# Kernel optimization log

Hardware: AMD Instinct MI355X
Metric: run time of the kernel (lower is better)

Reference implementation:

```python
import jax, jax.numpy as jnp
import numpy as np

HEAD_SIZE = 12
INNER_DIM = 64
BIG_NEG = 1e12


def _sinusoidal(seq_len, dim):
    # interleaved [sin, cos, sin, cos, ...] like SinusoidalPositionEmbedding('zero')
    pos = jnp.arange(seq_len, dtype=jnp.float32)
    inv = jnp.power(10000.0, -2.0 * jnp.arange(dim // 2, dtype=jnp.float32) / dim)
    ang = pos[:, None] * inv[None, :]                       # (L, dim/2)
    return jnp.stack([jnp.sin(ang), jnp.cos(ang)], axis=-1).reshape(seq_len, dim)


def _rope_rotate(x, cos_pos, sin_pos):
    # x: (B, L, H, D); rotate-half per interleaved RoPE
    x2 = jnp.stack([-x[..., 1::2], x[..., ::2]], axis=-1).reshape(x.shape)
    return x * cos_pos + x2 * sin_pos


def setup_inputs() -> dict:
    key = jax.random.key(0)
    k1, k2 = jax.random.split(key)
    B, L, HID = 16, 512, 768
    sequence_output = jax.random.normal(k1, (B, L, HID), dtype=jnp.float32)
    mask = jnp.ones((B, L), dtype=jnp.float32)
    W = jax.random.normal(k2, (HID, HEAD_SIZE * INNER_DIM * 2), dtype=jnp.float32) * 0.02
    b = jnp.zeros((HEAD_SIZE * INNER_DIM * 2,), dtype=jnp.float32)
    return {"sequence_output": sequence_output, "mask": mask, "W": W, "b": b}


def reference(sequence_output, mask, W, b):
    B, L, _ = sequence_output.shape
    H, D = HEAD_SIZE, INNER_DIM
    out = sequence_output @ W + b                           # (B, L, H*2D)
    out = out.reshape(B, L, H, 2 * D)
    qw, kw = out[..., :D], out[..., D:]                     # (B, L, H, D)
    pos = _sinusoidal(L, D)                                 # (L, D)
    cos_pos = jnp.repeat(pos[:, None, 1::2], 2, axis=-1)    # (L, 1, D)
    sin_pos = jnp.repeat(pos[:, None, ::2], 2, axis=-1)
    qw = _rope_rotate(qw, cos_pos, sin_pos)
    kw = _rope_rotate(kw, cos_pos, sin_pos)
    logits = jnp.einsum('bmhd,bnhd->bhmn', qw, kw)          # (B, H, L, L)
    pad = mask[:, None, None, :]                            # (B, 1, 1, L)
    logits = logits * pad - (1.0 - pad) * BIG_NEG
    tril = jnp.tril(jnp.ones((L, L), dtype=logits.dtype), -1)
    logits = logits - tril * BIG_NEG
    return logits / (D ** 0.5)
```

## Files before the change

### kernel.cpp

```cpp
#include <hip/hip_runtime.h>
#include <stdint.h>

typedef float f32x4 __attribute__((ext_vector_type(4)));

#define HEADS 12
#define DDIM 64
#define LSEQ 512
#define HID 768
#define NOUT 1536
#define BIG_NEG 1000000000000.0f

__device__ __forceinline__ void gl_lds16(const void* g, void* l) {
    __builtin_amdgcn_global_load_lds(
        (const __attribute__((address_space(1))) void*)g,
        (__attribute__((address_space(3))) void*)l, 16, 0, 0);
}

__device__ __forceinline__ void ldsbar() {
    asm volatile("s_waitcnt lgkmcnt(0)" ::: "memory");
    __builtin_amdgcn_s_barrier();
}

__device__ __forceinline__ uint32_t pk4_fp8(float a, float b, float c, float d) {
    uint32_t v = __builtin_amdgcn_cvt_pk_fp8_f32(a, b, 0, false);
    v = __builtin_amdgcn_cvt_pk_fp8_f32(c, d, v, true);
    return v;
}

__global__ __launch_bounds__(256) void prep_k(
    const float* __restrict__ X, const float* __restrict__ W,
    uint8_t* __restrict__ Xq, uint8_t* __restrict__ Wtq,
    float* __restrict__ cosT, float* __restrict__ sinT) {

    int blk = blockIdx.x;
    if (blk < 3072) {
        size_t idx = ((size_t)blk * 256 + threadIdx.x) * 8;
        float4 f0 = *(const float4*)(X + idx);
        float4 f1 = *(const float4*)(X + idx + 4);
        uint2 p;
        p.x = pk4_fp8(f0.x, f0.y, f0.z, f0.w);
        p.y = pk4_fp8(f1.x, f1.y, f1.z, f1.w);
        *(uint2*)(Xq + idx) = p;
    } else if (blk < 4224) {
        __shared__ float Ls[32][33];
        int b2 = blk - 3072;
        int n0 = (b2 % 48) * 32, k0 = (b2 / 48) * 32;
        int tx = threadIdx.x & 31, ty = threadIdx.x >> 5;
#pragma unroll
        for (int rr = 0; rr < 4; ++rr) {
            int k = ty + rr * 8;
            Ls[k][tx] = W[(size_t)(k0 + k) * NOUT + n0 + tx];
        }
        __syncthreads();
        int n = threadIdx.x >> 3, c = threadIdx.x & 7;
        uint32_t w = pk4_fp8(Ls[4*c][n], Ls[4*c+1][n], Ls[4*c+2][n], Ls[4*c+3][n]);
        *(uint32_t*)(Wtq + (size_t)(n0 + n) * HID + k0 + c * 4) = w;
    } else {
        int idx = (blk - 4224) * 256 + threadIdx.x;
        int l = idx >> 6, d = idx & 63;
        int p = d >> 1;
        float inv = powf(10000.0f, (-2.0f * (float)p) / 64.0f);
        float ang = (float)l * inv;
        cosT[idx] = cosf(ang);
        sinT[idx] = sinf(ang);
    }
}

__global__ __launch_bounds__(256) void proj_rope_k(
    const uint8_t* __restrict__ Xq, const uint8_t* __restrict__ Wtq,
    const float* __restrict__ bias, const float* __restrict__ cosT,
    const float* __restrict__ sinT,
    uint8_t* __restrict__ qq, uint8_t* __restrict__ kq) {

    __shared__ __align__(16) uint8_t As[128 * 64];
    __shared__ __align__(16) uint8_t Bs[128 * 64];

    const int tid = threadIdx.x;
    const int m0 = blockIdx.x * 128, n0 = blockIdx.y * 128;
    const int lane = tid & 63, wid = tid >> 6;
    const int wm = wid >> 1, wn = wid & 1;
    const int lr = lane & 15, kg = lane >> 4;

    const int srow = tid >> 2, sc = tid & 3;

    f32x4 acc[4][4] = {};

    for (int k0 = 0; k0 < HID; k0 += 64) {
#pragma unroll
        for (int j = 0; j < 2; ++j) {
            int r = j * 64 + srow;
            int cs = sc ^ ((r >> 1) & 3);
            gl_lds16(Wtq + (size_t)(n0 + r) * HID + k0 + cs * 16,
                     Bs + j * 4096 + tid * 16);
            gl_lds16(Xq + (size_t)(m0 + r) * HID + k0 + cs * 16,
                     As + j * 4096 + tid * 16);
        }
        __syncthreads();
#pragma unroll
        for (int ks = 0; ks < 2; ++ks) {
            unsigned long long af[4], xf[4];
#pragma unroll
            for (int ai = 0; ai < 4; ++ai) {
                int row = wn * 64 + ai * 16 + lr;
                int sl = (ks * 4 + kg) ^ (row & 6);
                af[ai] = *(const unsigned long long*)(Bs + row * 64 + sl * 8);
            }
#pragma unroll
            for (int bi = 0; bi < 4; ++bi) {
                int row = wm * 64 + bi * 16 + lr;
                int sl = (ks * 4 + kg) ^ (row & 6);
                xf[bi] = *(const unsigned long long*)(As + row * 64 + sl * 8);
            }
#pragma unroll
            for (int ai = 0; ai < 4; ++ai)
#pragma unroll
                for (int bi = 0; bi < 4; ++bi)
                    acc[ai][bi] = __builtin_amdgcn_mfma_f32_16x16x32_fp8_fp8(
                        (long long)af[ai], (long long)xf[bi], acc[ai][bi], 0, 0, 0);
        }
        __syncthreads();
    }

#pragma unroll
    for (int ai = 0; ai < 4; ++ai) {
        int nb = n0 + wn * 64 + ai * 16 + kg * 4;
        int h = nb >> 7, d2 = nb & 127;
        int d = d2 & 63;
        uint8_t* dst = (d2 >= 64) ? kq : qq;
        float4 b4 = *(const float4*)&bias[nb];
#pragma unroll
        for (int bi = 0; bi < 4; ++bi) {
            int m = m0 + wm * 64 + bi * 16 + lr;
            int bidx = m >> 9, lpos = m & 511;
            float4 c4 = *(const float4*)&cosT[lpos * 64 + d];
            float4 s4 = *(const float4*)&sinT[lpos * 64 + d];
            float v0 = acc[ai][bi][0] + b4.x;
            float v1 = acc[ai][bi][1] + b4.y;
            float v2 = acc[ai][bi][2] + b4.z;
            float v3 = acc[ai][bi][3] + b4.w;
            float o0 = v0 * c4.x - v1 * s4.x;
            float o1 = v1 * c4.y + v0 * s4.y;
            float o2 = v2 * c4.z - v3 * s4.z;
            float o3 = v3 * c4.w + v2 * s4.w;
            uint32_t pw = pk4_fp8(o0, o1, o2, o3);
            *(uint32_t*)(dst + (((size_t)bidx * HEADS + h) * LSEQ + lpos) * DDIM + d) = pw;
        }
    }
}

__global__ __launch_bounds__(256) void attn_k(
    const uint8_t* __restrict__ qq, const uint8_t* __restrict__ kq,
    const float* __restrict__ mask, float* __restrict__ out) {

    __shared__ __align__(16) uint8_t Qs[8192];
    __shared__ __align__(16) uint8_t Ks[8192];
    __shared__ __align__(16) float Es[32 * 132];
    __shared__ int wok[4];

    const int tid = threadIdx.x;
    const int bh = blockIdx.y;
    const int mtile = blockIdx.x;
    const int m0 = mtile * 128;
    const int lane = tid & 63, wid = tid >> 6;
    const int wm = wid >> 1, wn = wid & 1;
    const int lr = lane & 15, kg = lane >> 4;
    const int b = bh / HEADS;

    int myok = 1;
    for (int c0 = tid; c0 < m0; c0 += 256)
        myok &= (mask[b * LSEQ + c0] == 1.0f) ? 1 : 0;
    unsigned long long bal = __ballot(myok);
    if (lane == 0) wok[wid] = (bal == ~0ull) ? 1 : 0;
    ldsbar();
    const int nstart = (wok[0] & wok[1] & wok[2] & wok[3]) ? mtile : 0;

    const uint8_t* qbase = qq + ((size_t)bh * LSEQ + m0) * DDIM;
    const uint8_t* kbase = kq + (size_t)bh * LSEQ * DDIM;

    const int srow = tid >> 2, sc = tid & 3;
#pragma unroll
    for (int j = 0; j < 2; ++j) {
        int r = j * 64 + srow;
        int cs = sc ^ ((r >> 1) & 3);
        gl_lds16(qbase + (size_t)r * DDIM + cs * 16, Qs + j * 4096 + tid * 16);
        gl_lds16(kbase + (size_t)(nstart * 128 + r) * DDIM + cs * 16,
                 Ks + j * 4096 + tid * 16);
    }
    __syncthreads();

    const int colb = (tid & 31) * 4;
    const int rrow = tid >> 5;
    float* obase = out + (size_t)bh * LSEQ * LSEQ;

    for (int nt = nstart; nt < 4; ++nt) {
        f32x4 acc[4][4] = {};
#pragma unroll
        for (int ks = 0; ks < 2; ++ks) {
            unsigned long long af[4], qf[4];
#pragma unroll
            for (int ai = 0; ai < 4; ++ai) {
                int row = wn * 64 + ai * 16 + lr;
                int sl = (ks * 4 + kg) ^ (row & 6);
                af[ai] = *(const unsigned long long*)(Ks + row * 64 + sl * 8);
            }
#pragma unroll
            for (int bi = 0; bi < 4; ++bi) {
                int row = wm * 64 + bi * 16 + lr;
                int sl = (ks * 4 + kg) ^ (row & 6);
                qf[bi] = *(const unsigned long long*)(Qs + row * 64 + sl * 8);
            }
#pragma unroll
            for (int ai = 0; ai < 4; ++ai)
#pragma unroll
                for (int bi = 0; bi < 4; ++bi)
                    acc[ai][bi] = __builtin_amdgcn_mfma_f32_16x16x32_fp8_fp8(
                        (long long)af[ai], (long long)qf[bi], acc[ai][bi], 0, 0, 0);
        }
        ldsbar();

        const int n0 = nt * 128;
        const float4 p4 = *(const float4*)&mask[b * LSEQ + n0 + colb];

        if (nt < 3) {
#pragma unroll
            for (int j = 0; j < 2; ++j) {
                int r = j * 64 + srow;
                int cs = sc ^ ((r >> 1) & 3);
                gl_lds16(kbase + (size_t)((nt + 1) * 128 + r) * DDIM + cs * 16,
                         Ks + j * 4096 + tid * 16);
            }
        }

#pragma unroll
        for (int p = 0; p < 4; ++p) {
            ldsbar();
            if (wm == (p >> 1)) {
                const int bi0 = (p & 1) * 2;
#pragma unroll
                for (int bb = 0; bb < 2; ++bb) {
                    int bi = bi0 + bb;
                    int row = bb * 16 + lr;
#pragma unroll
                    for (int ai = 0; ai < 4; ++ai) {
                        int n = wn * 64 + ai * 16 + kg * 4;
                        *(f32x4*)&Es[row * 132 + n] = acc[ai][bi];
                    }
                }
            }
            ldsbar();
#pragma unroll
            for (int j = 0; j < 4; ++j) {
                int rloc = rrow + j * 8;
                int m = m0 + p * 32 + rloc;
                f32x4 v = *(f32x4*)&Es[rloc * 132 + colb];
                int n = n0 + colb;
                f32x4 o;
                o[0] = (v[0] * p4.x - (1.0f - p4.x) * BIG_NEG
                        - ((m > n + 0) ? BIG_NEG : 0.0f)) * 0.125f;
                o[1] = (v[1] * p4.y - (1.0f - p4.y) * BIG_NEG
                        - ((m > n + 1) ? BIG_NEG : 0.0f)) * 0.125f;
                o[2] = (v[2] * p4.z - (1.0f - p4.z) * BIG_NEG
                        - ((m > n + 2) ? BIG_NEG : 0.0f)) * 0.125f;
                o[3] = (v[3] * p4.w - (1.0f - p4.w) * BIG_NEG
                        - ((m > n + 3) ? BIG_NEG : 0.0f)) * 0.125f;
                __builtin_nontemporal_store(o, (f32x4*)&obase[(size_t)m * LSEQ + n]);
            }
        }

        if (nt < 3) {
            asm volatile("s_waitcnt vmcnt(16) lgkmcnt(0)" ::: "memory");
            __builtin_amdgcn_s_barrier();
        }
    }

    const float CONSTV = (-BIG_NEG) * 0.125f;
    f32x4 cv = {CONSTV, CONSTV, CONSTV, CONSTV};
    for (int nt2 = 0; nt2 < nstart; ++nt2) {
        int n = nt2 * 128 + colb;
#pragma unroll
        for (int p = 0; p < 4; ++p)
#pragma unroll
            for (int j = 0; j < 4; ++j) {
                int m = m0 + p * 32 + rrow + j * 8;
                __builtin_nontemporal_store(cv, (f32x4*)&obase[(size_t)m * LSEQ + n]);
            }
    }
}

extern "C" void kernel_launch(void* const* d_in, const int* in_sizes, int n_in,
                              void* d_out, int out_size, void* d_ws, size_t ws_size,
                              hipStream_t stream) {
    const float* X    = (const float*)d_in[0];
    const float* mask = (const float*)d_in[1];
    const float* W    = (const float*)d_in[2];
    const float* bias = (const float*)d_in[3];
    float* out = (float*)d_out;

    char* ws = (char*)d_ws;
    float*   cosT = (float*)ws;
    float*   sinT = (float*)(ws + 131072);
    uint8_t* Wtq  = (uint8_t*)(ws + 262144);
    uint8_t* Xq   = (uint8_t*)(ws + 1441792);
    uint8_t* qq   = (uint8_t*)(ws + 7733248);
    uint8_t* kq   = (uint8_t*)(ws + 14024704);

    prep_k<<<4352, 256, 0, stream>>>(X, W, Xq, Wtq, cosT, sinT);
    proj_rope_k<<<dim3(64, 12), 256, 0, stream>>>(Xq, Wtq, bias, cosT, sinT, qq, kq);
    attn_k<<<dim3(4, 192), 256, 0, stream>>>(qq, kq, mask, out);
}
```

Before: 86.63 us.

## Double-buffer projection GEMM and retile attention into 64-row blocks with remapped grid

The projection kernel now double-buffers its LDS tiles, prefetching the next K-slice while the MFMAs run on the current one. The attention kernel is retiled to 64 query rows per block, giving 1536 blocks with an XCD-aware index remap. Q fragments are loaded straight into registers instead of LDS, mask rows are preloaded, and the epilogue constants are folded into one FMA with a rotated Es layout to cut bank conflicts. The aim is better latency hiding and occupancy on the output-bandwidth-bound attention store, at the cost of more blocks, each reloading K tiles.

```diff
diff --git a/kernel.cpp b/kernel.cpp
--- a/kernel.cpp
+++ b/kernel.cpp
@@ -2,6 +2,7 @@
 #include <stdint.h>
 
 typedef float f32x4 __attribute__((ext_vector_type(4)));
+typedef unsigned long long u64;
 
 #define HEADS 12
 #define DDIM 64
@@ -9,6 +10,7 @@
 #define HID 768
 #define NOUT 1536
 #define BIG_NEG 1000000000000.0f
+#define BIGS 125000000000.0f
 
 __device__ __forceinline__ void gl_lds16(const void* g, void* l) {
     __builtin_amdgcn_global_load_lds(
@@ -72,8 +74,8 @@
     const float* __restrict__ sinT,
     uint8_t* __restrict__ qq, uint8_t* __restrict__ kq) {
 
-    __shared__ __align__(16) uint8_t As[128 * 64];
-    __shared__ __align__(16) uint8_t Bs[128 * 64];
+    __shared__ __align__(16) uint8_t As[2][128 * 64];
+    __shared__ __align__(16) uint8_t Bs[2][128 * 64];
 
     const int tid = threadIdx.x;
     const int m0 = blockIdx.x * 128, n0 = blockIdx.y * 128;
@@ -85,31 +87,47 @@
 
     f32x4 acc[4][4] = {};
 
-    for (int k0 = 0; k0 < HID; k0 += 64) {
-#pragma unroll
-        for (int j = 0; j < 2; ++j) {
-            int r = j * 64 + srow;
-            int cs = sc ^ ((r >> 1) & 3);
-            gl_lds16(Wtq + (size_t)(n0 + r) * HID + k0 + cs * 16,
-                     Bs + j * 4096 + tid * 16);
-            gl_lds16(Xq + (size_t)(m0 + r) * HID + k0 + cs * 16,
-                     As + j * 4096 + tid * 16);
-        }
-        __syncthreads();
+#pragma unroll
+    for (int j = 0; j < 2; ++j) {
+        int r = j * 64 + srow;
+        int cs = sc ^ ((r >> 1) & 3);
+        gl_lds16(Wtq + (size_t)(n0 + r) * HID + cs * 16, Bs[0] + j * 4096 + tid * 16);
+        gl_lds16(Xq  + (size_t)(m0 + r) * HID + cs * 16, As[0] + j * 4096 + tid * 16);
+    }
+
+    for (int it = 0; it < 12; ++it) {
+        const int cur = it & 1;
+        if (it < 11) {
+            const int k0 = (it + 1) * 64;
+#pragma unroll
+            for (int j = 0; j < 2; ++j) {
+                int r = j * 64 + srow;
+                int cs = sc ^ ((r >> 1) & 3);
+                gl_lds16(Wtq + (size_t)(n0 + r) * HID + k0 + cs * 16,
+                         Bs[cur ^ 1] + j * 4096 + tid * 16);
+                gl_lds16(Xq  + (size_t)(m0 + r) * HID + k0 + cs * 16,
+                         As[cur ^ 1] + j * 4096 + tid * 16);
+            }
+            asm volatile("s_waitcnt vmcnt(4)" ::: "memory");
+        } else {
+            asm volatile("s_waitcnt vmcnt(0)" ::: "memory");
+        }
+        __builtin_amdgcn_s_barrier();
+
 #pragma unroll
         for (int ks = 0; ks < 2; ++ks) {
-            unsigned long long af[4], xf[4];
+            u64 af[4], xf[4];
 #pragma unroll
             for (int ai = 0; ai < 4; ++ai) {
                 int row = wn * 64 + ai * 16 + lr;
                 int sl = (ks * 4 + kg) ^ (row & 6);
-                af[ai] = *(const unsigned long long*)(Bs + row * 64 + sl * 8);
+                af[ai] = *(const u64*)(Bs[cur] + row * 64 + sl * 8);
             }
 #pragma unroll
             for (int bi = 0; bi < 4; ++bi) {
                 int row = wm * 64 + bi * 16 + lr;
                 int sl = (ks * 4 + kg) ^ (row & 6);
-                xf[bi] = *(const unsigned long long*)(As + row * 64 + sl * 8);
+                xf[bi] = *(const u64*)(As[cur] + row * 64 + sl * 8);
             }
 #pragma unroll
             for (int ai = 0; ai < 4; ++ai)
@@ -118,7 +136,7 @@
                     acc[ai][bi] = __builtin_amdgcn_mfma_f32_16x16x32_fp8_fp8(
                         (long long)af[ai], (long long)xf[bi], acc[ai][bi], 0, 0, 0);
         }
-        __syncthreads();
+        ldsbar();
     }
 
 #pragma unroll
@@ -148,31 +166,31 @@
     }
 }
 
-__global__ __launch_bounds__(256) void attn_k(
+__global__ __launch_bounds__(256, 5) void attn_k(
     const uint8_t* __restrict__ qq, const uint8_t* __restrict__ kq,
     const float* __restrict__ mask, float* __restrict__ out) {
 
-    __shared__ __align__(16) uint8_t Qs[8192];
     __shared__ __align__(16) uint8_t Ks[8192];
     __shared__ __align__(16) float Es[32 * 132];
     __shared__ int wok[4];
 
     const int tid = threadIdx.x;
-    const int bh = blockIdx.y;
-    const int mtile = blockIdx.x;
-    const int m0 = mtile * 128;
-    const int lane = tid & 63, wid = tid >> 6;
-    const int wm = wid >> 1, wn = wid & 1;
+    const int bid = blockIdx.x;
+    const int L = (bid & 7) * 192 + (bid >> 3);
+    const int bh = L >> 3;
+    const int m0 = (L & 7) * 64;
+    const int lane = tid & 63, wn = tid >> 6;
     const int lr = lane & 15, kg = lane >> 4;
     const int b = bh / HEADS;
 
+    const int lim = m0 & ~127;
     int myok = 1;
-    for (int c0 = tid; c0 < m0; c0 += 256)
+    for (int c0 = tid; c0 < lim; c0 += 256)
         myok &= (mask[b * LSEQ + c0] == 1.0f) ? 1 : 0;
     unsigned long long bal = __ballot(myok);
-    if (lane == 0) wok[wid] = (bal == ~0ull) ? 1 : 0;
+    if (lane == 0) wok[wn] = (bal == ~0ull) ? 1 : 0;
     ldsbar();
-    const int nstart = (wok[0] & wok[1] & wok[2] & wok[3]) ? mtile : 0;
+    const int nstart = (wok[0] & wok[1] & wok[2] & wok[3]) ? (m0 >> 7) : 0;
 
     const uint8_t* qbase = qq + ((size_t)bh * LSEQ + m0) * DDIM;
     const uint8_t* kbase = kq + (size_t)bh * LSEQ * DDIM;
@@ -182,44 +200,48 @@
     for (int j = 0; j < 2; ++j) {
         int r = j * 64 + srow;
         int cs = sc ^ ((r >> 1) & 3);
-        gl_lds16(qbase + (size_t)r * DDIM + cs * 16, Qs + j * 4096 + tid * 16);
         gl_lds16(kbase + (size_t)(nstart * 128 + r) * DDIM + cs * 16,
                  Ks + j * 4096 + tid * 16);
     }
-    __syncthreads();
+
+    u64 qf[2][4];
+#pragma unroll
+    for (int ks = 0; ks < 2; ++ks)
+#pragma unroll
+        for (int bi = 0; bi < 4; ++bi)
+            qf[ks][bi] = *(const u64*)(qbase + (size_t)(bi * 16 + lr) * DDIM
+                                       + (ks * 4 + kg) * 8);
 
     const int colb = (tid & 31) * 4;
     const int rrow = tid >> 5;
+    float4 mrow[4];
+#pragma unroll
+    for (int t = 0; t < 4; ++t)
+        mrow[t] = *(const float4*)&mask[b * LSEQ + t * 128 + colb];
+
+    __syncthreads();
+
     float* obase = out + (size_t)bh * LSEQ * LSEQ;
 
     for (int nt = nstart; nt < 4; ++nt) {
-        f32x4 acc[4][4] = {};
+        f32x4 acc[2][4] = {};
 #pragma unroll
         for (int ks = 0; ks < 2; ++ks) {
-            unsigned long long af[4], qf[4];
-#pragma unroll
-            for (int ai = 0; ai < 4; ++ai) {
-                int row = wn * 64 + ai * 16 + lr;
+            u64 af[2];
+#pragma unroll
+            for (int ai = 0; ai < 2; ++ai) {
+                int row = wn * 32 + ai * 16 + lr;
                 int sl = (ks * 4 + kg) ^ (row & 6);
-                af[ai] = *(const unsigned long long*)(Ks + row * 64 + sl * 8);
-            }
-#pragma unroll
-            for (int bi = 0; bi < 4; ++bi) {
-                int row = wm * 64 + bi * 16 + lr;
-                int sl = (ks * 4 + kg) ^ (row & 6);
-                qf[bi] = *(const unsigned long long*)(Qs + row * 64 + sl * 8);
-            }
-#pragma unroll
-            for (int ai = 0; ai < 4; ++ai)
+                af[ai] = *(const u64*)(Ks + row * 64 + sl * 8);
+            }
+#pragma unroll
+            for (int ai = 0; ai < 2; ++ai)
 #pragma unroll
                 for (int bi = 0; bi < 4; ++bi)
                     acc[ai][bi] = __builtin_amdgcn_mfma_f32_16x16x32_fp8_fp8(
-                        (long long)af[ai], (long long)qf[bi], acc[ai][bi], 0, 0, 0);
+                        (long long)af[ai], (long long)qf[ks][bi], acc[ai][bi], 0, 0, 0);
         }
         ldsbar();
-
-        const int n0 = nt * 128;
-        const float4 p4 = *(const float4*)&mask[b * LSEQ + n0 + colb];
 
         if (nt < 3) {
 #pragma unroll
@@ -231,57 +253,56 @@
             }
         }
 
-#pragma unroll
-        for (int p = 0; p < 4; ++p) {
-            ldsbar();
-            if (wm == (p >> 1)) {
-                const int bi0 = (p & 1) * 2;
-#pragma unroll
-                for (int bb = 0; bb < 2; ++bb) {
-                    int bi = bi0 + bb;
-                    int row = bb * 16 + lr;
-#pragma unroll
-                    for (int ai = 0; ai < 4; ++ai) {
-                        int n = wn * 64 + ai * 16 + kg * 4;
-                        *(f32x4*)&Es[row * 132 + n] = acc[ai][bi];
-                    }
+        const float4 p4 = mrow[nt];
+        f32x4 ca = {p4.x * 0.125f, p4.y * 0.125f, p4.z * 0.125f, p4.w * 0.125f};
+        f32x4 cb = {(p4.x - 1.0f) * BIGS, (p4.y - 1.0f) * BIGS,
+                    (p4.z - 1.0f) * BIGS, (p4.w - 1.0f) * BIGS};
+        const int n0 = nt * 128;
+
+#pragma unroll
+        for (int p2 = 0; p2 < 2; ++p2) {
+#pragma unroll
+            for (int bb = 0; bb < 2; ++bb) {
+                int bi = p2 * 2 + bb;
+                int row = bb * 16 + lr;
+#pragma unroll
+                for (int ai = 0; ai < 2; ++ai) {
+                    int n = wn * 32 + ai * 16 + kg * 4;
+                    int nc = (n + row * 4) & 127;
+                    *(f32x4*)&Es[row * 132 + nc] = acc[ai][bi];
                 }
             }
             ldsbar();
 #pragma unroll
             for (int j = 0; j < 4; ++j) {
                 int rloc = rrow + j * 8;
-                int m = m0 + p * 32 + rloc;
-                f32x4 v = *(f32x4*)&Es[rloc * 132 + colb];
+                int nc = (colb + rloc * 4) & 127;
+                f32x4 v = *(f32x4*)&Es[rloc * 132 + nc];
+                int m = m0 + p2 * 32 + rloc;
                 int n = n0 + colb;
                 f32x4 o;
-                o[0] = (v[0] * p4.x - (1.0f - p4.x) * BIG_NEG
-                        - ((m > n + 0) ? BIG_NEG : 0.0f)) * 0.125f;
-                o[1] = (v[1] * p4.y - (1.0f - p4.y) * BIG_NEG
-                        - ((m > n + 1) ? BIG_NEG : 0.0f)) * 0.125f;
-                o[2] = (v[2] * p4.z - (1.0f - p4.z) * BIG_NEG
-                        - ((m > n + 2) ? BIG_NEG : 0.0f)) * 0.125f;
-                o[3] = (v[3] * p4.w - (1.0f - p4.w) * BIG_NEG
-                        - ((m > n + 3) ? BIG_NEG : 0.0f)) * 0.125f;
+#pragma unroll
+                for (int i = 0; i < 4; ++i)
+                    o[i] = v[i] * ca[i] + cb[i] - ((m > n + i) ? BIGS : 0.0f);
                 __builtin_nontemporal_store(o, (f32x4*)&obase[(size_t)m * LSEQ + n]);
             }
+            if (p2 == 0) ldsbar();
         }
 
         if (nt < 3) {
-            asm volatile("s_waitcnt vmcnt(16) lgkmcnt(0)" ::: "memory");
+            asm volatile("s_waitcnt vmcnt(8) lgkmcnt(0)" ::: "memory");
             __builtin_amdgcn_s_barrier();
         }
     }
 
-    const float CONSTV = (-BIG_NEG) * 0.125f;
-    f32x4 cv = {CONSTV, CONSTV, CONSTV, CONSTV};
+    f32x4 cv = {-BIGS, -BIGS, -BIGS, -BIGS};
     for (int nt2 = 0; nt2 < nstart; ++nt2) {
         int n = nt2 * 128 + colb;
 #pragma unroll
-        for (int p = 0; p < 4; ++p)
+        for (int p2 = 0; p2 < 2; ++p2)
 #pragma unroll
             for (int j = 0; j < 4; ++j) {
-                int m = m0 + p * 32 + rrow + j * 8;
+                int m = m0 + p2 * 32 + rrow + j * 8;
                 __builtin_nontemporal_store(cv, (f32x4*)&obase[(size_t)m * LSEQ + n]);
             }
     }
@@ -306,5 +327,5 @@
 
     prep_k<<<4352, 256, 0, stream>>>(X, W, Xq, Wtq, cosT, sinT);
     proj_rope_k<<<dim3(64, 12), 256, 0, stream>>>(Xq, Wtq, bias, cosT, sinT, qq, kq);
-    attn_k<<<dim3(4, 192), 256, 0, stream>>>(qq, kq, mask, out);
-}
+    attn_k<<<1536, 256, 0, stream>>>(qq, kq, mask, out);
+}
```

New measurement: 140.3 us. 62.0% more time.
